# Kernel optimization log

Measured on AMD Instinct MI355X. Metric: run time of the kernel, lower is better.

The kernel has to match this reference:

```python
import jax, jax.numpy as jnp
import numpy as np

N_NODES = 50000
N_EDGES = 800000
D_IN, D_HID, D_LAT = 96, 96, 64


def setup_inputs() -> dict:
    key = jax.random.key(0)
    ks = jax.random.split(key, 8)
    x = jax.random.normal(ks[0], (N_NODES, D_IN), dtype=jnp.float32)
    edge_index = jax.random.randint(ks[1], (2, N_EDGES), 0, N_NODES, dtype=jnp.int64)
    # Glorot-ish init for GCN weights, zero bias (PyG default bias=True)
    def glorot(k, fan_in, fan_out):
        s = jnp.sqrt(6.0 / (fan_in + fan_out))
        return jax.random.uniform(k, (fan_in, fan_out), jnp.float32, -s, s)
    return {
        "x": x,
        "edge_index": edge_index,
        "W0": glorot(ks[2], D_IN, D_HID), "b0": jnp.zeros((D_HID,), jnp.float32),
        "W1": glorot(ks[3], D_HID, D_HID), "b1": jnp.zeros((D_HID,), jnp.float32),
        "W2": glorot(ks[4], D_HID, D_LAT), "b2": jnp.zeros((D_LAT,), jnp.float32),
    }


def _gcn_layer(x, W, b, src, dst, dinv, n_nodes):
    # PyG GCNConv: h = x W; symmetric norm with self-loops; aggregate at dst; + bias
    h = x @ W  # [N, F_out]
    coef = dinv[src] * dinv[dst]                       # [E]
    msg = h[src] * coef[:, None]                       # gather + scale
    agg = jax.ops.segment_sum(msg, dst, num_segments=n_nodes)
    agg = agg + (dinv * dinv)[:, None] * h             # self-loop contribution
    return agg + b


def reference(x, edge_index, W0, b0, W1, b1, W2, b2):
    src, dst = edge_index[0], edge_index[1]
    n = x.shape[0]
    # degree at destination, +1 for the added self-loop (edge_weight = 1)
    deg = jax.ops.segment_sum(jnp.ones_like(dst, dtype=x.dtype), dst, num_segments=n) + 1.0
    dinv = deg ** -0.5
    h = jax.nn.relu(_gcn_layer(x, W0, b0, src, dst, dinv, n))
    h = jax.nn.relu(_gcn_layer(h, W1, b1, src, dst, dinv, n))
    mu = _gcn_layer(h, W2, b2, src, dst, dinv, n)
    logstd = mu  # module aliases logstd to mu
    return (mu, logstd)
```

## Files before the change

### kernel.cpp

```cpp
#include <hip/hip_runtime.h>
#include <hip/hip_fp16.h>

constexpr int NN = 50000;
constexpr int NE = 800000;
constexpr int NB = (NN + 1023) / 1024;

__global__ void k_count(const int* __restrict__ dst, int* __restrict__ cnt) {
    int e = blockIdx.x * blockDim.x + threadIdx.x;
    if (e < NE) atomicAdd(&cnt[dst[e]], 1);
}

__global__ void __launch_bounds__(1024) k_scanA(const int* __restrict__ cnt,
                                                int* __restrict__ rowptr,
                                                int* __restrict__ bsum,
                                                float* __restrict__ dinv) {
    __shared__ int wsum[16];
    int tid = threadIdx.x;
    int lane = tid & 63, wid = tid >> 6;
    int i = blockIdx.x * 1024 + tid;
    int v = (i < NN) ? cnt[i] : 0;
    int x = v;
#pragma unroll
    for (int off = 1; off < 64; off <<= 1) {
        int t = __shfl_up(x, off);
        if (lane >= off) x += t;
    }
    if (lane == 63) wsum[wid] = x;
    __syncthreads();
    if (wid == 0) {
        int wt = (lane < 16) ? wsum[lane] : 0;
        int y = wt;
#pragma unroll
        for (int off = 1; off < 16; off <<= 1) {
            int t = __shfl_up(y, off);
            if (lane >= off) y += t;
        }
        if (lane < 16) wsum[lane] = y - wt;
        if (lane == 15) bsum[blockIdx.x] = y;
    }
    __syncthreads();
    if (i < NN) {
        rowptr[i] = wsum[wid] + (x - v);
        dinv[i] = rsqrtf((float)v + 1.0f);
    }
}

__global__ void k_scanC(int* __restrict__ rowptr, const int* __restrict__ bsum,
                        int* __restrict__ cursor) {
    __shared__ int sboff[64];
    int tid = threadIdx.x;
    if (tid < 64) {
        int v = (tid < NB) ? bsum[tid] : 0;
        int x = v;
#pragma unroll
        for (int off = 1; off < 64; off <<= 1) {
            int t = __shfl_up(x, off);
            if (tid >= off) x += t;
        }
        sboff[tid] = x - v;
        if (blockIdx.x == 0 && tid == NB - 1) rowptr[NN] = x;
    }
    __syncthreads();
    int i = blockIdx.x * blockDim.x + tid;
    if (i < NN) {
        int r = rowptr[i] + sboff[i >> 10];
        rowptr[i] = r;
        cursor[i] = r;
    }
}

__global__ void k_fill(const int* __restrict__ src, const int* __restrict__ dst,
                       const float* __restrict__ dinv, int* __restrict__ cursor,
                       int2* __restrict__ pairs) {
    int e = blockIdx.x * blockDim.x + threadIdx.x;
    if (e >= NE) return;
    int s = src[e], d = dst[e];
    int pos = atomicAdd(&cursor[d], 1);
    float coef = dinv[s] * dinv[d];
    pairs[pos] = make_int2(s, __float_as_int(coef));
}

template<int FIN, int FOUT>
__global__ void k_gemm(const float* __restrict__ X, const float* __restrict__ W,
                       __half* __restrict__ H16) {
    constexpr int ROWS = 64, RPT = 4, CPT = 2;
    constexpr int GC = FOUT / 4;
    constexpr int CG = GC / CPT;
    constexpr int RG = ROWS / RPT;
    constexpr int NT = RG * CG;
    __shared__ float sW[FIN * FOUT];
    __shared__ float sX[ROWS * FIN];
    int tid = threadIdx.x;
    int row0 = blockIdx.x * ROWS;
    for (int i = tid; i < FIN * GC; i += NT)
        ((float4*)sW)[i] = ((const float4*)W)[i];
    constexpr int XF4 = ROWS * FIN / 4;
    for (int i = tid; i < XF4; i += NT) {
        int r = i / (FIN / 4);
        int gr = row0 + r;
        ((float4*)sX)[i] = (gr < NN)
            ? ((const float4*)(X + (size_t)gr * FIN))[i % (FIN / 4)]
            : make_float4(0.f, 0.f, 0.f, 0.f);
    }
    __syncthreads();
    int rg = tid / CG, cg = tid % CG;
    int rbase = rg * RPT;
    float4 acc[RPT][CPT] = {};
    for (int k = 0; k < FIN; k += 4) {
        float4 xv[RPT];
#pragma unroll
        for (int i = 0; i < RPT; ++i)
            xv[i] = *(const float4*)&sX[(rbase + i) * FIN + k];
#pragma unroll
        for (int kk = 0; kk < 4; ++kk) {
#pragma unroll
            for (int j = 0; j < CPT; ++j) {
                float4 w4 = ((const float4*)sW)[(k + kk) * GC + cg * CPT + j];
#pragma unroll
                for (int i = 0; i < RPT; ++i) {
                    float xs = (&xv[i].x)[kk];
                    acc[i][j].x += xs * w4.x; acc[i][j].y += xs * w4.y;
                    acc[i][j].z += xs * w4.z; acc[i][j].w += xs * w4.w;
                }
            }
        }
    }
#pragma unroll
    for (int i = 0; i < RPT; ++i) {
        int gr = row0 + rbase + i;
        if (gr < NN) {
            __half2 hp[4];
            hp[0] = __float22half2_rn(make_float2(acc[i][0].x, acc[i][0].y));
            hp[1] = __float22half2_rn(make_float2(acc[i][0].z, acc[i][0].w));
            hp[2] = __float22half2_rn(make_float2(acc[i][1].x, acc[i][1].y));
            hp[3] = __float22half2_rn(make_float2(acc[i][1].z, acc[i][1].w));
            ((float4*)H16)[(size_t)gr * (FOUT / 8) + cg] = *(float4*)hp;
        }
    }
}

template<int F, int MODE>
__global__ void k_agg(const __half* __restrict__ H16,
                      const int* __restrict__ rowptr, const int2* __restrict__ pairs,
                      const float* __restrict__ dinv, const float* __restrict__ b,
                      float* __restrict__ outp) {
    constexpr int C = F / 4;
    constexpr int T = F / 8;
    int tid = blockIdx.x * blockDim.x + threadIdx.x;
    int n = tid / T;
    int q = tid % T;
    if (n >= NN) return;
    int beg = rowptr[n], end = rowptr[n + 1];
    float di = dinv[n];
    const float4* g16 = (const float4*)H16;
    float4 a0 = make_float4(0.f, 0.f, 0.f, 0.f);
    float4 a1 = make_float4(0.f, 0.f, 0.f, 0.f);
#define ACC8(raw, cf)                                                          \
    {                                                                          \
        const __half2* hp_ = (const __half2*)&(raw);                           \
        float2 f0_ = __half22float2(hp_[0]); float2 f1_ = __half22float2(hp_[1]); \
        float2 f2_ = __half22float2(hp_[2]); float2 f3_ = __half22float2(hp_[3]); \
        a0.x += (cf) * f0_.x; a0.y += (cf) * f0_.y;                            \
        a0.z += (cf) * f1_.x; a0.w += (cf) * f1_.y;                            \
        a1.x += (cf) * f2_.x; a1.y += (cf) * f2_.y;                            \
        a1.z += (cf) * f3_.x; a1.w += (cf) * f3_.y;                            \
    }
    {
        float4 rs = g16[(size_t)n * T + q];
        ACC8(rs, di * di);
    }
    int p = beg;
    for (; p + 4 <= end; p += 4) {
        int2 e0 = pairs[p], e1 = pairs[p + 1], e2 = pairs[p + 2], e3 = pairs[p + 3];
        float4 r0 = g16[(size_t)e0.x * T + q];
        float4 r1 = g16[(size_t)e1.x * T + q];
        float4 r2 = g16[(size_t)e2.x * T + q];
        float4 r3 = g16[(size_t)e3.x * T + q];
        ACC8(r0, __int_as_float(e0.y));
        ACC8(r1, __int_as_float(e1.y));
        ACC8(r2, __int_as_float(e2.y));
        ACC8(r3, __int_as_float(e3.y));
    }
    for (; p < end; ++p) {
        int2 pr = pairs[p];
        float4 r = g16[(size_t)pr.x * T + q];
        ACC8(r, __int_as_float(pr.y));
    }
#undef ACC8
    float4 bb0 = *(const float4*)(b + q * 8);
    float4 bb1 = *(const float4*)(b + q * 8 + 4);
    a0.x += bb0.x; a0.y += bb0.y; a0.z += bb0.z; a0.w += bb0.w;
    a1.x += bb1.x; a1.y += bb1.y; a1.z += bb1.z; a1.w += bb1.w;
    size_t nb = (size_t)n * C + q * 2;
    if (MODE == 0) {
        a0.x = fmaxf(a0.x, 0.f); a0.y = fmaxf(a0.y, 0.f);
        a0.z = fmaxf(a0.z, 0.f); a0.w = fmaxf(a0.w, 0.f);
        a1.x = fmaxf(a1.x, 0.f); a1.y = fmaxf(a1.y, 0.f);
        a1.z = fmaxf(a1.z, 0.f); a1.w = fmaxf(a1.w, 0.f);
        ((float4*)outp)[nb] = a0;
        ((float4*)outp)[nb + 1] = a1;
    } else {
        ((float4*)outp)[nb] = a0;
        ((float4*)outp)[nb + 1] = a1;
        ((float4*)outp)[(size_t)NN * C + nb] = a0;
        ((float4*)outp)[(size_t)NN * C + nb + 1] = a1;
    }
}

extern "C" void kernel_launch(void* const* d_in, const int* in_sizes, int n_in,
                              void* d_out, int out_size, void* d_ws, size_t ws_size,
                              hipStream_t stream) {
    const float* x  = (const float*)d_in[0];
    const int*   ei = (const int*)d_in[1];
    const float* W0 = (const float*)d_in[2];
    const float* b0 = (const float*)d_in[3];
    const float* W1 = (const float*)d_in[4];
    const float* b1 = (const float*)d_in[5];
    const float* W2 = (const float*)d_in[6];
    const float* b2 = (const float*)d_in[7];
    float* out = (float*)d_out;

    int*    cnt    = (int*)d_ws;
    int*    rowptr = cnt + 51200;
    int*    cursor = rowptr + 51264;
    int*    bsum   = cursor + 51200;
    float*  dinv   = (float*)(bsum + 64);
    int2*   pairs  = (int2*)(dinv + 51200);
    float*  bufA   = (float*)(pairs + NE);
    __half* bufH16 = (__half*)(bufA + (size_t)NN * 96);

    const int* src = ei;
    const int* dst = ei + NE;

    hipMemsetAsync(cnt, 0, NN * sizeof(int), stream);
    k_count<<<NE / 256, 256, 0, stream>>>(dst, cnt);
    k_scanA<<<NB, 1024, 0, stream>>>(cnt, rowptr, bsum, dinv);
    k_scanC<<<(NN + 255) / 256, 256, 0, stream>>>(rowptr, bsum, cursor);
    k_fill<<<NE / 256, 256, 0, stream>>>(src, dst, dinv, cursor, pairs);

    constexpr int AG96 = (NN * 12 + 191) / 192;
    constexpr int AG64 = (NN * 8 + 191) / 192;
    constexpr int GEMMG = (NN + 63) / 64;

    k_gemm<96, 96><<<GEMMG, 192, 0, stream>>>(x, W0, bufH16);
    k_agg<96, 0><<<AG96, 192, 0, stream>>>(bufH16, rowptr, pairs, dinv, b0, bufA);
    k_gemm<96, 96><<<GEMMG, 192, 0, stream>>>(bufA, W1, bufH16);
    k_agg<96, 0><<<AG96, 192, 0, stream>>>(bufH16, rowptr, pairs, dinv, b1, bufA);
    k_gemm<96, 64><<<GEMMG, 128, 0, stream>>>(bufA, W2, bufH16);
    k_agg<64, 1><<<AG64, 192, 0, stream>>>(bufH16, rowptr, pairs, dinv, b2, out);
}
```

Measured before the change: 329.6 us.

## Transpose X tile in shared memory for GEMM and reuse rowptr as fill cursor

The GEMM now stores the input tile transposed in shared memory, so each thread loads one float4 holding four rows per k step. The output columns are interleaved across threads (cg + j*CG), which changes the half-precision stores to float2 writes. Separately, the CSR build drops the cursor array: k_fill bumps rowptr atomically, leaving each entry at its row's end, and k_agg reads beg from rowptr[n-1]. This removes one array write and read, but the transposed shared-memory stores may cause bank conflicts during the tile load.

```diff
diff --git a/kernel.cpp b/kernel.cpp
--- a/kernel.cpp
+++ b/kernel.cpp
@@ -45,8 +45,7 @@
     }
 }
 
-__global__ void k_scanC(int* __restrict__ rowptr, const int* __restrict__ bsum,
-                        int* __restrict__ cursor) {
+__global__ void k_scanC(int* __restrict__ rowptr, const int* __restrict__ bsum) {
     __shared__ int sboff[64];
     int tid = threadIdx.x;
     if (tid < 64) {
@@ -58,24 +57,19 @@
             if (tid >= off) x += t;
         }
         sboff[tid] = x - v;
-        if (blockIdx.x == 0 && tid == NB - 1) rowptr[NN] = x;
     }
     __syncthreads();
     int i = blockIdx.x * blockDim.x + tid;
-    if (i < NN) {
-        int r = rowptr[i] + sboff[i >> 10];
-        rowptr[i] = r;
-        cursor[i] = r;
-    }
+    if (i < NN) rowptr[i] += sboff[i >> 10];
 }
 
 __global__ void k_fill(const int* __restrict__ src, const int* __restrict__ dst,
-                       const float* __restrict__ dinv, int* __restrict__ cursor,
+                       const float* __restrict__ dinv, int* __restrict__ rowptr,
                        int2* __restrict__ pairs) {
     int e = blockIdx.x * blockDim.x + threadIdx.x;
     if (e >= NE) return;
     int s = src[e], d = dst[e];
-    int pos = atomicAdd(&cursor[d], 1);
+    int pos = atomicAdd(&rowptr[d], 1);
     float coef = dinv[s] * dinv[d];
     pairs[pos] = make_int2(s, __float_as_int(coef));
 }
@@ -89,39 +83,37 @@
     constexpr int RG = ROWS / RPT;
     constexpr int NT = RG * CG;
     __shared__ float sW[FIN * FOUT];
-    __shared__ float sX[ROWS * FIN];
+    __shared__ float sXT[FIN * ROWS];
     int tid = threadIdx.x;
     int row0 = blockIdx.x * ROWS;
     for (int i = tid; i < FIN * GC; i += NT)
         ((float4*)sW)[i] = ((const float4*)W)[i];
     constexpr int XF4 = ROWS * FIN / 4;
     for (int i = tid; i < XF4; i += NT) {
-        int r = i / (FIN / 4);
+        int r = i & 63;
+        int k4 = i >> 6;
         int gr = row0 + r;
-        ((float4*)sX)[i] = (gr < NN)
-            ? ((const float4*)(X + (size_t)gr * FIN))[i % (FIN / 4)]
-            : make_float4(0.f, 0.f, 0.f, 0.f);
+        float4 v = (gr < NN) ? ((const float4*)(X + (size_t)gr * FIN))[k4]
+                             : make_float4(0.f, 0.f, 0.f, 0.f);
+        sXT[(k4 * 4 + 0) * ROWS + r] = v.x;
+        sXT[(k4 * 4 + 1) * ROWS + r] = v.y;
+        sXT[(k4 * 4 + 2) * ROWS + r] = v.z;
+        sXT[(k4 * 4 + 3) * ROWS + r] = v.w;
     }
     __syncthreads();
     int rg = tid / CG, cg = tid % CG;
     int rbase = rg * RPT;
     float4 acc[RPT][CPT] = {};
-    for (int k = 0; k < FIN; k += 4) {
-        float4 xv[RPT];
-#pragma unroll
-        for (int i = 0; i < RPT; ++i)
-            xv[i] = *(const float4*)&sX[(rbase + i) * FIN + k];
-#pragma unroll
-        for (int kk = 0; kk < 4; ++kk) {
-#pragma unroll
-            for (int j = 0; j < CPT; ++j) {
-                float4 w4 = ((const float4*)sW)[(k + kk) * GC + cg * CPT + j];
-#pragma unroll
-                for (int i = 0; i < RPT; ++i) {
-                    float xs = (&xv[i].x)[kk];
-                    acc[i][j].x += xs * w4.x; acc[i][j].y += xs * w4.y;
-                    acc[i][j].z += xs * w4.z; acc[i][j].w += xs * w4.w;
-                }
+    for (int k = 0; k < FIN; ++k) {
+        float4 xk = *(const float4*)&sXT[k * ROWS + rbase];
+#pragma unroll
+        for (int j = 0; j < CPT; ++j) {
+            float4 w4 = ((const float4*)sW)[k * GC + cg + j * CG];
+#pragma unroll
+            for (int i = 0; i < RPT; ++i) {
+                float xs = (&xk.x)[i];
+                acc[i][j].x += xs * w4.x; acc[i][j].y += xs * w4.y;
+                acc[i][j].z += xs * w4.z; acc[i][j].w += xs * w4.w;
             }
         }
     }
@@ -129,12 +121,13 @@
     for (int i = 0; i < RPT; ++i) {
         int gr = row0 + rbase + i;
         if (gr < NN) {
-            __half2 hp[4];
-            hp[0] = __float22half2_rn(make_float2(acc[i][0].x, acc[i][0].y));
-            hp[1] = __float22half2_rn(make_float2(acc[i][0].z, acc[i][0].w));
-            hp[2] = __float22half2_rn(make_float2(acc[i][1].x, acc[i][1].y));
-            hp[3] = __float22half2_rn(make_float2(acc[i][1].z, acc[i][1].w));
-            ((float4*)H16)[(size_t)gr * (FOUT / 8) + cg] = *(float4*)hp;
+#pragma unroll
+            for (int j = 0; j < CPT; ++j) {
+                float2 pk;
+                ((__half2*)&pk)[0] = __float22half2_rn(make_float2(acc[i][j].x, acc[i][j].y));
+                ((__half2*)&pk)[1] = __float22half2_rn(make_float2(acc[i][j].z, acc[i][j].w));
+                ((float2*)(H16 + (size_t)gr * FOUT))[cg + j * CG] = pk;
+            }
         }
     }
 }
@@ -150,7 +143,8 @@
     int n = tid / T;
     int q = tid % T;
     if (n >= NN) return;
-    int beg = rowptr[n], end = rowptr[n + 1];
+    int beg = (n > 0) ? rowptr[n - 1] : 0;
+    int end = rowptr[n];
     float di = dinv[n];
     const float4* g16 = (const float4*)H16;
     float4 a0 = make_float4(0.f, 0.f, 0.f, 0.f);
@@ -222,8 +216,7 @@
 
     int*    cnt    = (int*)d_ws;
     int*    rowptr = cnt + 51200;
-    int*    cursor = rowptr + 51264;
-    int*    bsum   = cursor + 51200;
+    int*    bsum   = rowptr + 51264;
     float*  dinv   = (float*)(bsum + 64);
     int2*   pairs  = (int2*)(dinv + 51200);
     float*  bufA   = (float*)(pairs + NE);
@@ -235,8 +228,8 @@
     hipMemsetAsync(cnt, 0, NN * sizeof(int), stream);
     k_count<<<NE / 256, 256, 0, stream>>>(dst, cnt);
     k_scanA<<<NB, 1024, 0, stream>>>(cnt, rowptr, bsum, dinv);
-    k_scanC<<<(NN + 255) / 256, 256, 0, stream>>>(rowptr, bsum, cursor);
-    k_fill<<<NE / 256, 256, 0, stream>>>(src, dst, dinv, cursor, pairs);
+    k_scanC<<<(NN + 255) / 256, 256, 0, stream>>>(rowptr, bsum);
+    k_fill<<<NE / 256, 256, 0, stream>>>(src, dst, dinv, rowptr, pairs);
 
     constexpr int AG96 = (NN * 12 + 191) / 192;
     constexpr int AG64 = (NN * 8 + 191) / 192;
```

Result: no change. 323.3 us (-1.9%).
